# Kernel tuning notes

Hardware: AMD Instinct MI355X
Metric: run time of the kernel (lower is better)

Reference implementation:

```python
import jax, jax.numpy as jnp
import numpy as np


def setup_inputs() -> dict:
    key = jax.random.key(0)
    x = jax.random.normal(key, (32, 1, 1024, 1024), dtype=jnp.float32)
    return {"x": x}


def reference(x) -> jnp.ndarray:
    # Original torch loop computes a running max down the height dim (dim=2)
    # for channel 0 (C=1 here), overwriting each element with the prefix max.
    # This is exactly a cumulative-max (prefix-max scan) along axis=2.
    return jax.lax.associative_scan(jnp.maximum, x, axis=2)
```

## Files before the change

### kernel.cpp

```cpp
#include <hip/hip_runtime.h>


constexpr int B = 32;
constexpr int H = 1024;
constexpr int W = 1024;
constexpr int SWF = 64;
constexpr int NSTRIP = W / SWF;
constexpr int NBLK = B * NSTRIP;
constexpr int D = 32;
static_assert(H % D == 0, "D must divide H");

__global__ __launch_bounds__(64) void cummax_stream(const float* __restrict__ x,
                                                    float* __restrict__ o) {
    const int sid = blockIdx.x;
    const int b = sid >> 4;
    const int st = sid & (NSTRIP - 1);
    const int lane = threadIdx.x;

    const size_t base = (size_t)b * H * W + (size_t)st * SWF + lane;
    const float* xp = x + base;
    float* op = o + base;

    float carry = -__builtin_inff();
    float buf[D];

#pragma unroll
    for (int r = 0; r < D; ++r) buf[r] = xp[(size_t)r * W];

    int hb = 0;
    for (; hb < H - D; hb += D) {
        const float* xn = xp + (size_t)(hb + D) * W;
        float* on = op + (size_t)hb * W;
#pragma unroll
        for (int r = 0; r < D; ++r) {
            float v = buf[r];
            buf[r] = xn[(size_t)r * W];
            carry = fmaxf(carry, v);
            on[(size_t)r * W] = carry;
        }
    }

    {
        float* on = op + (size_t)hb * W;
#pragma unroll
        for (int r = 0; r < D; ++r) {
            carry = fmaxf(carry, buf[r]);
            on[(size_t)r * W] = carry;
        }
    }
}

extern "C" void kernel_launch(void* const* d_in, const int* in_sizes, int n_in,
                              void* d_out, int out_size, void* d_ws, size_t ws_size,
                              hipStream_t stream) {
    const float* x = (const float*)d_in[0];
    float* out = (float*)d_out;
    cummax_stream<<<NBLK, 64, 0, stream>>>(x, out);
}
```

Before: 235.1 us.

## Split prefix-max into band column-max reduce and band apply passes

Replaces the single serial column-strip scan with a two-kernel reduce-then-scan: the first kernel computes per-band column maxima into workspace, the second combines preceding band aggregates as a carry and rescans its band writing outputs. Uses float4 accesses and many more blocks to expose parallelism and memory-level concurrency. It costs an extra full read of the input and requires a workspace, falling back to the old kernel otherwise.

```diff
diff --git a/kernel.cpp b/kernel.cpp
--- a/kernel.cpp
+++ b/kernel.cpp
@@ -4,6 +4,101 @@
 constexpr int B = 32;
 constexpr int H = 1024;
 constexpr int W = 1024;
+constexpr int ROW4 = W / 4;
+constexpr int NSEG = 32;
+constexpr int SH = H / NSEG;
+constexpr int NB = B * NSEG;
+constexpr size_t AGG_BYTES = (size_t)NB * ROW4 * sizeof(float4);
+
+__device__ __forceinline__ float4 max4(float4 a, float4 b) {
+    return make_float4(fmaxf(a.x, b.x), fmaxf(a.y, b.y),
+                       fmaxf(a.z, b.z), fmaxf(a.w, b.w));
+}
+
+__global__ __launch_bounds__(256) void band_colmax(const float* __restrict__ xf,
+                                                   float* __restrict__ tf) {
+    const int id = blockIdx.x;
+    const int b = id >> 5;
+    const int s = id & (NSEG - 1);
+    const int t = threadIdx.x;
+    const float4* x4 = (const float4*)xf;
+    float4* t4 = (float4*)tf;
+
+    const size_t base = ((size_t)b * H + (size_t)s * SH) * ROW4 + t;
+
+    float4 cur[8], nxt[8];
+#pragma unroll
+    for (int r = 0; r < 8; ++r) cur[r] = x4[base + (size_t)r * ROW4];
+
+    const float ninf = -__builtin_inff();
+    float4 m = make_float4(ninf, ninf, ninf, ninf);
+
+#pragma unroll
+    for (int g = 0; g < SH; g += 8) {
+        if (g + 8 < SH) {
+#pragma unroll
+            for (int r = 0; r < 8; ++r)
+                nxt[r] = x4[base + (size_t)(g + 8 + r) * ROW4];
+        }
+#pragma unroll
+        for (int r = 0; r < 8; ++r) m = max4(m, cur[r]);
+        if (g + 8 < SH) {
+#pragma unroll
+            for (int r = 0; r < 8; ++r) cur[r] = nxt[r];
+        }
+    }
+    t4[(size_t)id * ROW4 + t] = m;
+}
+
+__global__ __launch_bounds__(256) void band_apply(const float* __restrict__ xf,
+                                                  const float* __restrict__ tf,
+                                                  float* __restrict__ of) {
+    const int id = blockIdx.x;
+    const int b = id >> 5;
+    const int s = id & (NSEG - 1);
+    const int t = threadIdx.x;
+    const float4* x4 = (const float4*)xf;
+    const float4* t4 = (const float4*)tf;
+    float4* o4 = (float4*)of;
+
+    const float ninf = -__builtin_inff();
+    float4 carry = make_float4(ninf, ninf, ninf, ninf);
+
+    for (int g = 0; g < s; g += 8) {
+        float4 v[8];
+#pragma unroll
+        for (int k = 0; k < 8; ++k)
+            v[k] = t4[(size_t)(b * NSEG + g + k) * ROW4 + t];
+#pragma unroll
+        for (int k = 0; k < 8; ++k)
+            if (g + k < s) carry = max4(carry, v[k]);
+    }
+
+    const size_t base = ((size_t)b * H + (size_t)s * SH) * ROW4 + t;
+
+    float4 cur[8], nxt[8];
+#pragma unroll
+    for (int r = 0; r < 8; ++r) cur[r] = x4[base + (size_t)r * ROW4];
+
+#pragma unroll
+    for (int g = 0; g < SH; g += 8) {
+        if (g + 8 < SH) {
+#pragma unroll
+            for (int r = 0; r < 8; ++r)
+                nxt[r] = x4[base + (size_t)(g + 8 + r) * ROW4];
+        }
+#pragma unroll
+        for (int r = 0; r < 8; ++r) {
+            carry = max4(carry, cur[r]);
+            o4[base + (size_t)(g + r) * ROW4] = carry;
+        }
+        if (g + 8 < SH) {
+#pragma unroll
+            for (int r = 0; r < 8; ++r) cur[r] = nxt[r];
+        }
+    }
+}
+
 constexpr int SWF = 64;
 constexpr int NSTRIP = W / SWF;
 constexpr int NBLK = B * NSTRIP;
@@ -16,17 +111,13 @@
     const int b = sid >> 4;
     const int st = sid & (NSTRIP - 1);
     const int lane = threadIdx.x;
-
     const size_t base = (size_t)b * H * W + (size_t)st * SWF + lane;
     const float* xp = x + base;
     float* op = o + base;
-
     float carry = -__builtin_inff();
     float buf[D];
-
 #pragma unroll
     for (int r = 0; r < D; ++r) buf[r] = xp[(size_t)r * W];
-
     int hb = 0;
     for (; hb < H - D; hb += D) {
         const float* xn = xp + (size_t)(hb + D) * W;
@@ -39,7 +130,6 @@
             on[(size_t)r * W] = carry;
         }
     }
-
     {
         float* on = op + (size_t)hb * W;
 #pragma unroll
@@ -55,5 +145,11 @@
                               hipStream_t stream) {
     const float* x = (const float*)d_in[0];
     float* out = (float*)d_out;
-    cummax_stream<<<NBLK, 64, 0, stream>>>(x, out);
+    if (d_ws != nullptr && ws_size >= AGG_BYTES) {
+        float* agg = (float*)d_ws;
+        band_colmax<<<NB, 256, 0, stream>>>(x, agg);
+        band_apply<<<NB, 256, 0, stream>>>(x, agg, out);
+    } else {
+        cummax_stream<<<NBLK, 64, 0, stream>>>(x, out);
+    }
 }
```

Measured after the change: 258.3 us. 9.9% more time.
